# Performance work log

Hardware: AMD Instinct MI355X
Metric: run time of the kernel (lower is better)

The kernel has to match this reference:

```python
import jax, jax.numpy as jnp
import numpy as np

B, T, I, O = 128, 512, 700, 128  # batch, nb_steps, input_size, output_size
TIME_STEP, TAU_SYN, TAU_MEM, GAMMA_SHAPE = 1e-3, 10e-3, 20e-3, 3.0


def setup_inputs() -> dict:
    key = jax.random.key(0)
    k1, k2 = jax.random.split(key)
    inputs = jax.random.normal(k1, (B, T, I), dtype=jnp.float32)
    bound = 1.0 / np.sqrt(I)  # kaiming-uniform-like fan_in bound
    w = jax.random.uniform(k2, (I, O), minval=-bound, maxval=bound, dtype=jnp.float32)
    # heterogeneous per-neuron decay constants (het_ab=True), frozen params
    rng = np.random.default_rng(0)
    alpha = jnp.asarray(np.exp(-TIME_STEP / rng.gamma(GAMMA_SHAPE, TAU_SYN / GAMMA_SHAPE, (1, O))), dtype=jnp.float32)
    beta = jnp.asarray(np.exp(-TIME_STEP / rng.gamma(GAMMA_SHAPE, TAU_MEM / GAMMA_SHAPE, (1, O))), dtype=jnp.float32)
    return {"inputs": inputs, "w": w, "alpha": alpha, "beta": beta}


def reference(inputs, w, alpha, beta):
    # h: (B, T, O)
    h = jnp.einsum('btc,cd->btd', inputs, w)
    Bh, Th, Oh = h.shape
    zeros = jnp.zeros((Bh, Oh), dtype=h.dtype)
    one_minus_beta = 1.0 - beta  # beta is frozen, detach is a no-op here

    def step(carry, ht):
        syn, mem = carry
        new_syn = alpha * syn + ht
        new_mem = beta * mem + one_minus_beta * syn  # uses OLD syn
        return (new_syn, new_mem), (new_syn, new_mem)

    # scan over the first T-1 timesteps (time-major)
    h_tm = jnp.swapaxes(h[:, :Th - 1], 0, 1)  # (T-1, B, O)
    _, (syn_seq, mem_seq) = jax.lax.scan(step, (zeros, zeros), h_tm)
    syn_rec = jnp.concatenate([zeros[:, None], jnp.swapaxes(syn_seq, 0, 1)], axis=1)  # (B, T, O)
    mem_rec = jnp.concatenate([zeros[:, None], jnp.swapaxes(mem_seq, 0, 1)], axis=1)
    return (syn_rec, mem_rec)
```

## Files before the change

### kernel.cpp

```cpp
#include <hip/hip_runtime.h>
#include <hip/hip_bf16.h>
#include <stdint.h>

#define Bsz 128
#define Tn  512
#define In  700
#define On  128
#define Mn  (Bsz * Tn)
#define KP  704
#define NSEG 16
#define LSEG 32
#define BO   (Bsz * On)
#define NKT  22

using bf16x8 = __attribute__((ext_vector_type(8))) short;
using f32x4  = __attribute__((ext_vector_type(4))) float;

#define WAITVM(N) asm volatile("s_waitcnt vmcnt(" #N ")" ::: "memory")

__device__ __forceinline__ uint32_t f2bf(float f) {
  union { float f; uint32_t u; } v; v.f = f;
  return (v.u + 0x7fffu + ((v.u >> 16) & 1u)) >> 16;
}

__device__ __forceinline__ bf16x8 cvt8(float4 f0, float4 f1) {
  union { __hip_bfloat162 h2[4]; bf16x8 v; } u;
  u.h2[0] = __float22bfloat162_rn(make_float2(f0.x, f0.y));
  u.h2[1] = __float22bfloat162_rn(make_float2(f0.z, f0.w));
  u.h2[2] = __float22bfloat162_rn(make_float2(f1.x, f1.y));
  u.h2[3] = __float22bfloat162_rn(make_float2(f1.z, f1.w));
  return u.v;
}

__device__ __forceinline__ void gload16(const void* g, void* l) {
  __builtin_amdgcn_global_load_lds(
      (__attribute__((address_space(1))) void*)g,
      (__attribute__((address_space(3))) void*)l, 16, 0, 0);
}

__global__ void prep_wt(const float* __restrict__ w, ushort* __restrict__ w_t) {
  int idx = blockIdx.x * 256 + threadIdx.x;
  if (idx >= On * KP) return;
  int col = idx / KP, k = idx - col * KP;
  float v = (k < In) ? w[(size_t)k * On + col] : 0.0f;
  w_t[(size_t)col * KP + k] = (ushort)f2bf(v);
}

union SMU {
  struct {
    uint32_t A[3][4096];
    uint32_t B[3][2048];
  } db;
  float sc[128 * 132];
};

__global__ __launch_bounds__(256, 2) void gemm_h(
    const float* __restrict__ A,
    const ushort* __restrict__ Wt,
    float* __restrict__ H,
    float2* __restrict__ ep,
    const float* __restrict__ alpha, const float* __restrict__ beta)
{
  __shared__ __align__(16) SMU sm;

  const int tid  = threadIdx.x;
  const int bm   = blockIdx.x;
  const int lane = tid & 63;
  const int wid  = tid >> 6;
  const int wm   = wid >> 1, wn = wid & 1;
  const int l16  = lane & 15, lkb = lane >> 4;

  const int   o_ep = tid & 127;
  const float a_ep = alpha[o_ep];
  const float b_ep = beta[o_ep];
  WAITVM(0);
  __builtin_amdgcn_sched_barrier(0);

  f32x4 acc[4][4];
#pragma unroll
  for (int i = 0; i < 4; ++i)
#pragma unroll
    for (int n = 0; n < 4; ++n) acc[i][n] = (f32x4){0.f, 0.f, 0.f, 0.f};

  auto stage = [&](int bi, int kt) {
    const int k0 = kt * 32;
#pragma unroll
    for (int is = 0; is < 4; ++is) {
      const int q   = is * 256 + wid * 64 + lane;
      const int row = q >> 3, sl = q & 7;
      int gk = k0 + ((sl ^ (row & 7)) << 2);
      if (gk >= In) gk = k0;
      gload16(A + (size_t)(bm * 128 + row) * In + gk,
              &sm.db.A[bi][is * 1024 + wid * 256]);
    }
#pragma unroll
    for (int is = 0; is < 2; ++is) {
      const int q   = is * 256 + wid * 64 + lane;
      const int col = q >> 2, sl = q & 3;
      const int ks  = sl ^ ((col >> 1) & 3);
      gload16(Wt + (size_t)col * KP + k0 + ks * 8,
              &sm.db.B[bi][is * 1024 + wid * 256]);
    }
  };

  auto tile = [&](int kt, int cur) {
    __builtin_amdgcn_s_barrier();
    const float4* Af = (const float4*)sm.db.A[cur];
    const bf16x8* Bf = (const bf16x8*)sm.db.B[cur];
    bf16x8 af[4], bfr[4];
#pragma unroll
    for (int i = 0; i < 4; ++i) {
      const int row = wm * 64 + i * 16 + l16;
      const int s0  = (lkb * 2) ^ (row & 7);
      const int s1  = (lkb * 2 + 1) ^ (row & 7);
      af[i] = cvt8(Af[row * 8 + s0], Af[row * 8 + s1]);
    }
#pragma unroll
    for (int n = 0; n < 4; ++n) {
      const int col = wn * 64 + n * 16 + l16;
      bfr[n] = Bf[col * 4 + (lkb ^ ((col >> 1) & 3))];
    }
    asm volatile("s_waitcnt lgkmcnt(0)" ::: "memory");
    __builtin_amdgcn_s_barrier();
    if (kt + 3 < NKT) stage(cur, kt + 3);
#pragma unroll
    for (int i = 0; i < 4; ++i)
#pragma unroll
      for (int n = 0; n < 4; ++n)
        acc[i][n] = __builtin_amdgcn_mfma_f32_16x16x32_bf16(af[i], bfr[n], acc[i][n], 0, 0, 0);
  };

  stage(0, 0); stage(1, 1); stage(2, 2);
  {
    int cur = 0;
    for (int kt = 0; kt < NKT - 2; ++kt) {
      WAITVM(12);
      tile(kt, cur);
      cur = (cur == 2) ? 0 : cur + 1;
    }
    WAITVM(6);  tile(NKT - 2, (NKT - 2) % 3);
    WAITVM(0);  tile(NKT - 1, (NKT - 1) % 3);
  }

#pragma unroll
  for (int i = 0; i < 4; ++i)
#pragma unroll
    for (int n = 0; n < 4; ++n) {
      const int col = wn * 64 + n * 16 + l16;
#pragma unroll
      for (int r = 0; r < 4; ++r) {
        const int row = wm * 64 + i * 16 + lkb * 4 + r;
        sm.sc[row * 132 + col] = acc[i][n][r];
      }
    }
  __syncthreads();

  const size_t hbase = (size_t)bm * 128 * 128;
#pragma unroll
  for (int i2 = 0; i2 < 16; ++i2) {
    const int q = i2 * 256 + tid;
    const int row = q >> 5, v = q & 31;
    *(float4*)&H[hbase + row * 128 + v * 4] =
        *(const float4*)&sm.sc[row * 132 + v * 4];
  }

  if (ep) {
    const float a = a_ep, bt = b_ep, omb = 1.0f - b_ep;
    const int b = bm >> 2, seg0 = (bm & 3) * 4;
#pragma unroll
    for (int cc = 0; cc < 2; ++cc) {
      const int sl = (tid >> 7) + cc * 2;
      float S = 0.f, M = 0.f;
      const float* base = &sm.sc[(sl * 32) * 132 + o_ep];
#pragma unroll
      for (int t = 0; t < 32; ++t) {
        const float x = base[t * 132];
        M = fmaf(bt, M, omb * S);
        S = fmaf(a, S, x);
      }
      ep[(size_t)(seg0 + sl) * BO + b * On + o_ep] = make_float2(S, M);
    }
  }
}

__global__ __launch_bounds__(256) void scan_seg(
    float* __restrict__ syn, float* __restrict__ mem, const float2* __restrict__ ep,
    const float* __restrict__ alpha, const float* __restrict__ beta)
{
  const int cid = blockIdx.x * 256 + threadIdx.x;
  const int o2  = cid & 63;
  const int seg = (cid >> 6) & (NSEG - 1);
  const int b   = cid >> 10;
  const int o   = 2 * o2;

  const float2 al2 = *(const float2*)&alpha[o];
  const float2 be2 = *(const float2*)&beta[o];
  const float a0 = al2.x, a1 = al2.y, b0 = be2.x, b1 = be2.y;
  const float ob0 = 1.f - b0, ob1 = 1.f - b1;

  float aL0 = 1.f, bL0 = 1.f, cL0 = 0.f, aL1 = 1.f, bL1 = 1.f, cL1 = 0.f;
#pragma unroll
  for (int i = 0; i < LSEG; ++i) {
    cL0 = fmaf(b0, cL0, ob0 * aL0); aL0 *= a0; bL0 *= b0;
    cL1 = fmaf(b1, cL1, ob1 * aL1); aL1 *= a1; bL1 *= b1;
  }

  float S0 = 0.f, M0 = 0.f, S1 = 0.f, M1 = 0.f;
  for (int j = 0; j < seg; ++j) {
    const float4 E = *(const float4*)&ep[(size_t)j * BO + b * On + o];
    const float nS0 = fmaf(aL0, S0, E.x);
    M0 = fmaf(bL0, M0, fmaf(cL0, S0, E.y));
    S0 = nS0;
    const float nS1 = fmaf(aL1, S1, E.z);
    M1 = fmaf(bL1, M1, fmaf(cL1, S1, E.w));
    S1 = nS1;
  }

  float* hp = syn + ((size_t)b * Tn + seg * LSEG) * On + o;
  float* mp = mem + ((size_t)b * Tn + seg * LSEG) * On + o;
  float2 buf[8];
#pragma unroll
  for (int d = 0; d < 8; ++d) buf[d] = *(const float2*)&hp[d * On];
  for (int tb = 0; tb < LSEG; tb += 8) {
#pragma unroll
    for (int d = 0; d < 8; ++d) {
      const int t = tb + d;
      const float2 x = buf[d];
      if (t + 8 < LSEG) buf[d] = *(const float2*)&hp[(t + 8) * On];
      *(float2*)&hp[(size_t)t * On] = make_float2(S0, S1);
      *(float2*)&mp[(size_t)t * On] = make_float2(M0, M1);
      M0 = fmaf(b0, M0, ob0 * S0); S0 = fmaf(a0, S0, x.x);
      M1 = fmaf(b1, M1, ob1 * S1); S1 = fmaf(a1, S1, x.y);
    }
  }
}

__global__ __launch_bounds__(64) void scan_k(
    float* __restrict__ syn, float* __restrict__ mem,
    const float* __restrict__ alpha, const float* __restrict__ beta)
{
  const int b = blockIdx.x >> 1;
  const int o = ((blockIdx.x & 1) << 6) + threadIdx.x;
  const float a = alpha[o], bt = beta[o], omb = 1.0f - bt;
  float* hp = syn + (size_t)b * Tn * On + o;
  float* mp = mem + (size_t)b * Tn * On + o;
  float S = 0.f, M = 0.f;
  float buf[8];
#pragma unroll
  for (int d = 0; d < 8; ++d) buf[d] = hp[d * On];
  for (int tb = 0; tb < Tn; tb += 8) {
#pragma unroll
    for (int d = 0; d < 8; ++d) {
      const int t = tb + d;
      const float h_t = buf[d];
      if (t + 8 < Tn) buf[d] = hp[(t + 8) * On];
      hp[t * On] = S;
      mp[t * On] = M;
      const float nS = fmaf(a, S, h_t);
      M = fmaf(bt, M, omb * S);
      S = nS;
    }
  }
}

extern "C" void kernel_launch(void* const* d_in, const int* in_sizes, int n_in,
                              void* d_out, int out_size, void* d_ws, size_t ws_size,
                              hipStream_t stream) {
  const float* inputs = (const float*)d_in[0];
  const float* w      = (const float*)d_in[1];
  const float* alpha  = (const float*)d_in[2];
  const float* beta   = (const float*)d_in[3];

  float* syn = (float*)d_out;
  float* mem = syn + (size_t)Bsz * Tn * On;
  ushort* w_t = (ushort*)mem;

  const size_t ep_bytes = (size_t)NSEG * BO * sizeof(float2);
  float2* ep = (ws_size >= ep_bytes) ? (float2*)d_ws : nullptr;

  prep_wt<<<(On * KP + 255) / 256, 256, 0, stream>>>(w, w_t);
  gemm_h<<<Mn / 128, 256, 0, stream>>>(inputs, w_t, syn, ep, alpha, beta);

  if (ep) {
    scan_seg<<<(Bsz * NSEG * On / 2) / 256, 256, 0, stream>>>(syn, mem, ep, alpha, beta);
  } else {
    scan_k<<<Bsz * 2, 64, 0, stream>>>(syn, mem, alpha, beta);
  }
}
```

Baseline: 62.13 us.

## Store GEMM intermediate h as bf16 in workspace and scan from it

The GEMM now rounds its h tile to bf16 and writes it as packed bf16 to a workspace buffer instead of fp32 into the syn output. A new scan kernel reads the bf16 h, processes four output columns per thread, and writes syn and mem. The segment-boundary summaries are also computed from the rounded values, so the intermediate traffic for h is halved. In exchange, h carries bf16 rounding, which adds error to syn and mem, and the path needs a larger workspace.

```diff
diff --git a/kernel.cpp b/kernel.cpp
--- a/kernel.cpp
+++ b/kernel.cpp
@@ -22,6 +22,18 @@
   union { float f; uint32_t u; } v; v.f = f;
   return (v.u + 0x7fffu + ((v.u >> 16) & 1u)) >> 16;
 }
+__device__ __forceinline__ float bf16exact(float x) {
+  union { float f; uint32_t u; } v; v.f = x;
+  v.u = (v.u + 0x7fffu + ((v.u >> 16) & 1u)) & 0xFFFF0000u;
+  return v.f;
+}
+__device__ __forceinline__ float bf2f(ushort u) {
+  union { float f; uint32_t x; } v; v.x = ((uint32_t)u) << 16;
+  return v.f;
+}
+__device__ __forceinline__ uint32_t topbits(float x) {
+  union { float f; uint32_t u; } v; v.f = x; return v.u;
+}
 
 __device__ __forceinline__ bf16x8 cvt8(float4 f0, float4 f1) {
   union { __hip_bfloat162 h2[4]; bf16x8 v; } u;
@@ -54,10 +66,12 @@
   float sc[128 * 132];
 };
 
+template <bool HB16>
 __global__ __launch_bounds__(256, 2) void gemm_h(
     const float* __restrict__ A,
     const ushort* __restrict__ Wt,
-    float* __restrict__ H,
+    float* __restrict__ Hf,
+    ushort* __restrict__ Hb,
     float2* __restrict__ ep,
     const float* __restrict__ alpha, const float* __restrict__ beta)
 {
@@ -150,18 +164,36 @@
 #pragma unroll
       for (int r = 0; r < 4; ++r) {
         const int row = wm * 64 + i * 16 + lkb * 4 + r;
-        sm.sc[row * 132 + col] = acc[i][n][r];
+        float v = acc[i][n][r];
+        if constexpr (HB16) v = bf16exact(v);
+        sm.sc[row * 132 + col] = v;
       }
     }
   __syncthreads();
 
-  const size_t hbase = (size_t)bm * 128 * 128;
-#pragma unroll
-  for (int i2 = 0; i2 < 16; ++i2) {
-    const int q = i2 * 256 + tid;
-    const int row = q >> 5, v = q & 31;
-    *(float4*)&H[hbase + row * 128 + v * 4] =
-        *(const float4*)&sm.sc[row * 132 + v * 4];
+  if constexpr (HB16) {
+#pragma unroll
+    for (int i2 = 0; i2 < 8; ++i2) {
+      const int q = i2 * 256 + tid;
+      const int row = q >> 4, v8 = q & 15;
+      const float4 f0 = *(const float4*)&sm.sc[row * 132 + v8 * 8];
+      const float4 f1 = *(const float4*)&sm.sc[row * 132 + v8 * 8 + 4];
+      uint4 pk;
+      pk.x = (topbits(f0.x) >> 16) | (topbits(f0.y) & 0xFFFF0000u);
+      pk.y = (topbits(f0.z) >> 16) | (topbits(f0.w) & 0xFFFF0000u);
+      pk.z = (topbits(f1.x) >> 16) | (topbits(f1.y) & 0xFFFF0000u);
+      pk.w = (topbits(f1.z) >> 16) | (topbits(f1.w) & 0xFFFF0000u);
+      *(uint4*)&Hb[(size_t)(bm * 128 + row) * 128 + v8 * 8] = pk;
+    }
+  } else {
+    const size_t hbase = (size_t)bm * 128 * 128;
+#pragma unroll
+    for (int i2 = 0; i2 < 16; ++i2) {
+      const int q = i2 * 256 + tid;
+      const int row = q >> 5, v = q & 31;
+      *(float4*)&Hf[hbase + row * 128 + v * 4] =
+          *(const float4*)&sm.sc[row * 132 + v * 4];
+    }
   }
 
   if (ep) {
@@ -179,6 +211,72 @@
         S = fmaf(a, S, x);
       }
       ep[(size_t)(seg0 + sl) * BO + b * On + o_ep] = make_float2(S, M);
+    }
+  }
+}
+
+__global__ __launch_bounds__(256) void scan_seg16(
+    float* __restrict__ syn, float* __restrict__ mem,
+    const ushort* __restrict__ Hb, const float2* __restrict__ ep,
+    const float* __restrict__ alpha, const float* __restrict__ beta)
+{
+  const int cid = blockIdx.x * 256 + threadIdx.x;
+  const int o4  = cid & 31;
+  const int seg = (cid >> 5) & (NSEG - 1);
+  const int b   = cid >> 9;
+  const int o   = o4 * 4;
+
+  const float4 al = *(const float4*)&alpha[o];
+  const float4 be = *(const float4*)&beta[o];
+  float aa[4] = {al.x, al.y, al.z, al.w};
+  float bb[4] = {be.x, be.y, be.z, be.w};
+  float ob[4], aL[4], bL[4], cL[4], S[4], M[4];
+#pragma unroll
+  for (int c = 0; c < 4; ++c) {
+    ob[c] = 1.f - bb[c]; aL[c] = 1.f; bL[c] = 1.f; cL[c] = 0.f;
+    S[c] = 0.f; M[c] = 0.f;
+  }
+#pragma unroll
+  for (int i = 0; i < LSEG; ++i)
+#pragma unroll
+    for (int c = 0; c < 4; ++c) {
+      cL[c] = fmaf(bb[c], cL[c], ob[c] * aL[c]);
+      aL[c] *= aa[c]; bL[c] *= bb[c];
+    }
+
+  for (int j = 0; j < seg; ++j) {
+    const float4 E0 = *(const float4*)&ep[(size_t)j * BO + b * On + o];
+    const float4 E1 = *(const float4*)&ep[(size_t)j * BO + b * On + o + 2];
+    const float ex[4] = {E0.x, E0.z, E1.x, E1.z};
+    const float ey[4] = {E0.y, E0.w, E1.y, E1.w};
+#pragma unroll
+    for (int c = 0; c < 4; ++c) {
+      const float nS = fmaf(aL[c], S[c], ex[c]);
+      M[c] = fmaf(bL[c], M[c], fmaf(cL[c], S[c], ey[c]));
+      S[c] = nS;
+    }
+  }
+
+  const ushort* hp = Hb + ((size_t)b * Tn + seg * LSEG) * On + o;
+  float* sp = syn + ((size_t)b * Tn + seg * LSEG) * On + o;
+  float* mp = mem + ((size_t)b * Tn + seg * LSEG) * On + o;
+  ushort4 buf[4];
+#pragma unroll
+  for (int d = 0; d < 4; ++d) buf[d] = *(const ushort4*)&hp[d * On];
+  for (int tb = 0; tb < LSEG; tb += 4) {
+#pragma unroll
+    for (int d = 0; d < 4; ++d) {
+      const int t = tb + d;
+      const ushort4 u = buf[d];
+      if (t + 4 < LSEG) buf[d] = *(const ushort4*)&hp[(t + 4) * On];
+      *(float4*)&sp[(size_t)t * On] = make_float4(S[0], S[1], S[2], S[3]);
+      *(float4*)&mp[(size_t)t * On] = make_float4(M[0], M[1], M[2], M[3]);
+      const float x[4] = {bf2f(u.x), bf2f(u.y), bf2f(u.z), bf2f(u.w)};
+#pragma unroll
+      for (int c = 0; c < 4; ++c) {
+        M[c] = fmaf(bb[c], M[c], ob[c] * S[c]);
+        S[c] = fmaf(aa[c], S[c], x[c]);
+      }
     }
   }
 }
@@ -276,14 +374,21 @@
   ushort* w_t = (ushort*)mem;
 
   const size_t ep_bytes = (size_t)NSEG * BO * sizeof(float2);
-  float2* ep = (ws_size >= ep_bytes) ? (float2*)d_ws : nullptr;
+  const size_t hb_bytes = (size_t)Mn * On * sizeof(ushort);
 
   prep_wt<<<(On * KP + 255) / 256, 256, 0, stream>>>(w, w_t);
-  gemm_h<<<Mn / 128, 256, 0, stream>>>(inputs, w_t, syn, ep, alpha, beta);
-
-  if (ep) {
+
+  if (ws_size >= ep_bytes + hb_bytes) {
+    float2* ep = (float2*)d_ws;
+    ushort* hb = (ushort*)((char*)d_ws + ep_bytes);
+    gemm_h<true><<<Mn / 128, 256, 0, stream>>>(inputs, w_t, nullptr, hb, ep, alpha, beta);
+    scan_seg16<<<(Bsz * NSEG * On / 4) / 256, 256, 0, stream>>>(syn, mem, hb, ep, alpha, beta);
+  } else if (ws_size >= ep_bytes) {
+    float2* ep = (float2*)d_ws;
+    gemm_h<false><<<Mn / 128, 256, 0, stream>>>(inputs, w_t, syn, nullptr, ep, alpha, beta);
     scan_seg<<<(Bsz * NSEG * On / 2) / 256, 256, 0, stream>>>(syn, mem, ep, alpha, beta);
   } else {
+    gemm_h<false><<<Mn / 128, 256, 0, stream>>>(inputs, w_t, syn, nullptr, nullptr, alpha, beta);
     scan_k<<<Bsz * 2, 64, 0, stream>>>(syn, mem, alpha, beta);
   }
 }
```

Result: no change. 63.37 us (+2.0%).

## Load GEMM operands directly to registers and pass H as bf16 to the scan

Applied to the files above, without the earlier changes.

The GEMM drops the LDS triple-buffered global_load_lds staging and instead double-buffers A and W tiles in registers, with each wave computing 32 rows by all 128 columns. When the workspace is large enough, the intermediate H is rounded to bf16 and written to a workspace buffer instead of fp32 into the syn output. A new scan kernel then reads the half-size bf16 H. This cuts intermediate write and read traffic, at the cost of bf16 precision in the scan input and possibly weaker load coalescing or reuse in the GEMM without LDS sharing.

```diff
diff --git a/kernel.cpp b/kernel.cpp
--- a/kernel.cpp
+++ b/kernel.cpp
@@ -16,11 +16,20 @@
 using bf16x8 = __attribute__((ext_vector_type(8))) short;
 using f32x4  = __attribute__((ext_vector_type(4))) float;
 
-#define WAITVM(N) asm volatile("s_waitcnt vmcnt(" #N ")" ::: "memory")
-
 __device__ __forceinline__ uint32_t f2bf(float f) {
   union { float f; uint32_t u; } v; v.f = f;
   return (v.u + 0x7fffu + ((v.u >> 16) & 1u)) >> 16;
+}
+__device__ __forceinline__ float bf16exact(float x) {
+  union { float f; uint32_t u; } v; v.f = x;
+  v.u = (v.u + 0x7fffu + ((v.u >> 16) & 1u)) & 0xFFFF0000u;
+  return v.f;
+}
+__device__ __forceinline__ float bitsf(uint32_t u) {
+  union { float f; uint32_t x; } v; v.x = u; return v.f;
+}
+__device__ __forceinline__ uint32_t topbits(float x) {
+  union { float f; uint32_t u; } v; v.f = x; return v.u;
 }
 
 __device__ __forceinline__ bf16x8 cvt8(float4 f0, float4 f1) {
@@ -32,12 +41,6 @@
   return u.v;
 }
 
-__device__ __forceinline__ void gload16(const void* g, void* l) {
-  __builtin_amdgcn_global_load_lds(
-      (__attribute__((address_space(1))) void*)g,
-      (__attribute__((address_space(3))) void*)l, 16, 0, 0);
-}
-
 __global__ void prep_wt(const float* __restrict__ w, ushort* __restrict__ w_t) {
   int idx = blockIdx.x * 256 + threadIdx.x;
   if (idx >= On * KP) return;
@@ -46,122 +49,111 @@
   w_t[(size_t)col * KP + k] = (ushort)f2bf(v);
 }
 
-union SMU {
-  struct {
-    uint32_t A[3][4096];
-    uint32_t B[3][2048];
-  } db;
-  float sc[128 * 132];
-};
-
-__global__ __launch_bounds__(256, 2) void gemm_h(
+template <bool HB16>
+__global__ __launch_bounds__(256, 2) void gemm_h2(
     const float* __restrict__ A,
     const ushort* __restrict__ Wt,
-    float* __restrict__ H,
+    float* __restrict__ Hf,
+    ushort* __restrict__ Hb,
     float2* __restrict__ ep,
     const float* __restrict__ alpha, const float* __restrict__ beta)
 {
-  __shared__ __align__(16) SMU sm;
+  __shared__ float sc[128 * 132];
 
   const int tid  = threadIdx.x;
   const int bm   = blockIdx.x;
   const int lane = tid & 63;
-  const int wid  = tid >> 6;
-  const int wm   = wid >> 1, wn = wid & 1;
+  const int w    = tid >> 6;
   const int l16  = lane & 15, lkb = lane >> 4;
 
   const int   o_ep = tid & 127;
   const float a_ep = alpha[o_ep];
   const float b_ep = beta[o_ep];
-  WAITVM(0);
-  __builtin_amdgcn_sched_barrier(0);
-
-  f32x4 acc[4][4];
-#pragma unroll
-  for (int i = 0; i < 4; ++i)
-#pragma unroll
-    for (int n = 0; n < 4; ++n) acc[i][n] = (f32x4){0.f, 0.f, 0.f, 0.f};
-
-  auto stage = [&](int bi, int kt) {
+
+  const float*  ap0 = A + (size_t)(bm * 128 + w * 32 + l16) * In + lkb * 8;
+  const float*  ap1 = ap0 + (size_t)16 * In;
+  const ushort* wp  = Wt + (size_t)l16 * KP + lkb * 8;
+
+  f32x4 acc[2][8];
+#pragma unroll
+  for (int m = 0; m < 2; ++m)
+#pragma unroll
+    for (int n = 0; n < 8; ++n) acc[m][n] = (f32x4){0.f, 0.f, 0.f, 0.f};
+
+  struct Tile { float4 a00, a01, a10, a11; bf16x8 b[8]; };
+  auto loadT = [&](int kt, Tile& T) {
     const int k0 = kt * 32;
-#pragma unroll
-    for (int is = 0; is < 4; ++is) {
-      const int q   = is * 256 + wid * 64 + lane;
-      const int row = q >> 3, sl = q & 7;
-      int gk = k0 + ((sl ^ (row & 7)) << 2);
-      if (gk >= In) gk = k0;
-      gload16(A + (size_t)(bm * 128 + row) * In + gk,
-              &sm.db.A[bi][is * 1024 + wid * 256]);
-    }
-#pragma unroll
-    for (int is = 0; is < 2; ++is) {
-      const int q   = is * 256 + wid * 64 + lane;
-      const int col = q >> 2, sl = q & 3;
-      const int ks  = sl ^ ((col >> 1) & 3);
-      gload16(Wt + (size_t)col * KP + k0 + ks * 8,
-              &sm.db.B[bi][is * 1024 + wid * 256]);
-    }
+    const int gk = k0;
+    const int d2 = (k0 + lkb * 8 + 4 <= In - 4) ? 4 : (In - 4 - (k0 + lkb * 8));
+    T.a00 = *(const float4*)(ap0 + gk);
+    T.a01 = *(const float4*)(ap0 + gk + d2);
+    T.a10 = *(const float4*)(ap1 + gk);
+    T.a11 = *(const float4*)(ap1 + gk + d2);
+#pragma unroll
+    for (int n = 0; n < 8; ++n)
+      T.b[n] = *(const bf16x8*)(wp + (size_t)n * 16 * KP + k0);
   };
-
-  auto tile = [&](int kt, int cur) {
-    __builtin_amdgcn_s_barrier();
-    const float4* Af = (const float4*)sm.db.A[cur];
-    const bf16x8* Bf = (const bf16x8*)sm.db.B[cur];
-    bf16x8 af[4], bfr[4];
-#pragma unroll
-    for (int i = 0; i < 4; ++i) {
-      const int row = wm * 64 + i * 16 + l16;
-      const int s0  = (lkb * 2) ^ (row & 7);
-      const int s1  = (lkb * 2 + 1) ^ (row & 7);
-      af[i] = cvt8(Af[row * 8 + s0], Af[row * 8 + s1]);
-    }
-#pragma unroll
-    for (int n = 0; n < 4; ++n) {
-      const int col = wn * 64 + n * 16 + l16;
-      bfr[n] = Bf[col * 4 + (lkb ^ ((col >> 1) & 3))];
-    }
-    asm volatile("s_waitcnt lgkmcnt(0)" ::: "memory");
-    __builtin_amdgcn_s_barrier();
-    if (kt + 3 < NKT) stage(cur, kt + 3);
-#pragma unroll
-    for (int i = 0; i < 4; ++i)
-#pragma unroll
-      for (int n = 0; n < 4; ++n)
-        acc[i][n] = __builtin_amdgcn_mfma_f32_16x16x32_bf16(af[i], bfr[n], acc[i][n], 0, 0, 0);
+  auto compute = [&](const Tile& T) {
+    bf16x8 af0 = cvt8(T.a00, T.a01);
+    bf16x8 af1 = cvt8(T.a10, T.a11);
+#pragma unroll
+    for (int n = 0; n < 8; ++n) {
+      acc[0][n] = __builtin_amdgcn_mfma_f32_16x16x32_bf16(af0, T.b[n], acc[0][n], 0, 0, 0);
+      acc[1][n] = __builtin_amdgcn_mfma_f32_16x16x32_bf16(af1, T.b[n], acc[1][n], 0, 0, 0);
+    }
   };
 
-  stage(0, 0); stage(1, 1); stage(2, 2);
-  {
-    int cur = 0;
-    for (int kt = 0; kt < NKT - 2; ++kt) {
-      WAITVM(12);
-      tile(kt, cur);
-      cur = (cur == 2) ? 0 : cur + 1;
-    }
-    WAITVM(6);  tile(NKT - 2, (NKT - 2) % 3);
-    WAITVM(0);  tile(NKT - 1, (NKT - 1) % 3);
-  }
-
-#pragma unroll
-  for (int i = 0; i < 4; ++i)
-#pragma unroll
-    for (int n = 0; n < 4; ++n) {
-      const int col = wn * 64 + n * 16 + l16;
+  Tile R0, R1;
+  loadT(0, R0);
+#pragma unroll 1
+  for (int kt = 0; kt < NKT - 2; kt += 2) {
+    loadT(kt + 1, R1);
+    compute(R0);
+    loadT(kt + 2, R0);
+    compute(R1);
+  }
+  loadT(NKT - 1, R1);
+  compute(R0);
+  compute(R1);
+
+#pragma unroll
+  for (int m = 0; m < 2; ++m)
+#pragma unroll
+    for (int n = 0; n < 8; ++n) {
+      const int col = n * 16 + l16;
 #pragma unroll
       for (int r = 0; r < 4; ++r) {
-        const int row = wm * 64 + i * 16 + lkb * 4 + r;
-        sm.sc[row * 132 + col] = acc[i][n][r];
+        const int row = w * 32 + m * 16 + lkb * 4 + r;
+        float v = acc[m][n][r];
+        if constexpr (HB16) v = bf16exact(v);
+        sc[row * 132 + col] = v;
       }
     }
   __syncthreads();
 
-  const size_t hbase = (size_t)bm * 128 * 128;
-#pragma unroll
-  for (int i2 = 0; i2 < 16; ++i2) {
-    const int q = i2 * 256 + tid;
-    const int row = q >> 5, v = q & 31;
-    *(float4*)&H[hbase + row * 128 + v * 4] =
-        *(const float4*)&sm.sc[row * 132 + v * 4];
+  if constexpr (HB16) {
+#pragma unroll
+    for (int i2 = 0; i2 < 8; ++i2) {
+      const int q = i2 * 256 + tid;
+      const int row = q >> 4, v8 = q & 15;
+      const float4 f0 = *(const float4*)&sc[row * 132 + v8 * 8];
+      const float4 f1 = *(const float4*)&sc[row * 132 + v8 * 8 + 4];
+      uint4 pk;
+      pk.x = (topbits(f0.x) >> 16) | (topbits(f0.y) & 0xFFFF0000u);
+      pk.y = (topbits(f0.z) >> 16) | (topbits(f0.w) & 0xFFFF0000u);
+      pk.z = (topbits(f1.x) >> 16) | (topbits(f1.y) & 0xFFFF0000u);
+      pk.w = (topbits(f1.z) >> 16) | (topbits(f1.w) & 0xFFFF0000u);
+      *(uint4*)&Hb[(size_t)(bm * 128 + row) * 128 + v8 * 8] = pk;
+    }
+  } else {
+    const size_t hbase = (size_t)bm * 128 * 128;
+#pragma unroll
+    for (int i2 = 0; i2 < 16; ++i2) {
+      const int q = i2 * 256 + tid;
+      const int row = q >> 5, v = q & 31;
+      *(float4*)&Hf[hbase + row * 128 + v * 4] =
+          *(const float4*)&sc[row * 132 + v * 4];
+    }
   }
 
   if (ep) {
@@ -171,7 +163,7 @@
     for (int cc = 0; cc < 2; ++cc) {
       const int sl = (tid >> 7) + cc * 2;
       float S = 0.f, M = 0.f;
-      const float* base = &sm.sc[(sl * 32) * 132 + o_ep];
+      const float* base = &sc[(sl * 32) * 132 + o_ep];
 #pragma unroll
       for (int t = 0; t < 32; ++t) {
         const float x = base[t * 132];
@@ -179,6 +171,62 @@
         S = fmaf(a, S, x);
       }
       ep[(size_t)(seg0 + sl) * BO + b * On + o_ep] = make_float2(S, M);
+    }
+  }
+}
+
+__global__ __launch_bounds__(256) void scan_segb(
+    float* __restrict__ syn, float* __restrict__ mem,
+    const ushort* __restrict__ Hb, const float2* __restrict__ ep,
+    const float* __restrict__ alpha, const float* __restrict__ beta)
+{
+  const int cid = blockIdx.x * 256 + threadIdx.x;
+  const int o2  = cid & 63;
+  const int seg = (cid >> 6) & (NSEG - 1);
+  const int b   = cid >> 10;
+  const int o   = 2 * o2;
+
+  const float2 al2 = *(const float2*)&alpha[o];
+  const float2 be2 = *(const float2*)&beta[o];
+  const float a0 = al2.x, a1 = al2.y, b0 = be2.x, b1 = be2.y;
+  const float ob0 = 1.f - b0, ob1 = 1.f - b1;
+
+  float aL0 = 1.f, bL0 = 1.f, cL0 = 0.f, aL1 = 1.f, bL1 = 1.f, cL1 = 0.f;
+#pragma unroll
+  for (int i = 0; i < LSEG; ++i) {
+    cL0 = fmaf(b0, cL0, ob0 * aL0); aL0 *= a0; bL0 *= b0;
+    cL1 = fmaf(b1, cL1, ob1 * aL1); aL1 *= a1; bL1 *= b1;
+  }
+
+  float S0 = 0.f, M0 = 0.f, S1 = 0.f, M1 = 0.f;
+  for (int j = 0; j < seg; ++j) {
+    const float4 E = *(const float4*)&ep[(size_t)j * BO + b * On + o];
+    const float nS0 = fmaf(aL0, S0, E.x);
+    M0 = fmaf(bL0, M0, fmaf(cL0, S0, E.y));
+    S0 = nS0;
+    const float nS1 = fmaf(aL1, S1, E.z);
+    M1 = fmaf(bL1, M1, fmaf(cL1, S1, E.w));
+    S1 = nS1;
+  }
+
+  const ushort* hp = Hb + ((size_t)b * Tn + seg * LSEG) * On + o;
+  float* sp = syn + ((size_t)b * Tn + seg * LSEG) * On + o;
+  float* mp = mem + ((size_t)b * Tn + seg * LSEG) * On + o;
+  uint32_t buf[8];
+#pragma unroll
+  for (int d = 0; d < 8; ++d) buf[d] = *(const uint32_t*)&hp[d * On];
+  for (int tb = 0; tb < LSEG; tb += 8) {
+#pragma unroll
+    for (int d = 0; d < 8; ++d) {
+      const int t = tb + d;
+      const uint32_t u = buf[d];
+      if (t + 8 < LSEG) buf[d] = *(const uint32_t*)&hp[(t + 8) * On];
+      *(float2*)&sp[(size_t)t * On] = make_float2(S0, S1);
+      *(float2*)&mp[(size_t)t * On] = make_float2(M0, M1);
+      const float x0 = bitsf(u << 16);
+      const float x1 = bitsf(u & 0xFFFF0000u);
+      M0 = fmaf(b0, M0, ob0 * S0); S0 = fmaf(a0, S0, x0);
+      M1 = fmaf(b1, M1, ob1 * S1); S1 = fmaf(a1, S1, x1);
     }
   }
 }
@@ -276,14 +324,21 @@
   ushort* w_t = (ushort*)mem;
 
   const size_t ep_bytes = (size_t)NSEG * BO * sizeof(float2);
-  float2* ep = (ws_size >= ep_bytes) ? (float2*)d_ws : nullptr;
+  const size_t hb_bytes = (size_t)Mn * On * sizeof(ushort);
 
   prep_wt<<<(On * KP + 255) / 256, 256, 0, stream>>>(w, w_t);
-  gemm_h<<<Mn / 128, 256, 0, stream>>>(inputs, w_t, syn, ep, alpha, beta);
-
-  if (ep) {
+
+  if (ws_size >= ep_bytes + hb_bytes) {
+    float2* ep = (float2*)d_ws;
+    ushort* hb = (ushort*)((char*)d_ws + ep_bytes);
+    gemm_h2<true><<<Mn / 128, 256, 0, stream>>>(inputs, w_t, nullptr, hb, ep, alpha, beta);
+    scan_segb<<<(Bsz * NSEG * On / 2) / 256, 256, 0, stream>>>(syn, mem, hb, ep, alpha, beta);
+  } else if (ws_size >= ep_bytes) {
+    float2* ep = (float2*)d_ws;
+    gemm_h2<false><<<Mn / 128, 256, 0, stream>>>(inputs, w_t, syn, nullptr, ep, alpha, beta);
     scan_seg<<<(Bsz * NSEG * On / 2) / 256, 256, 0, stream>>>(syn, mem, ep, alpha, beta);
   } else {
+    gemm_h2<false><<<Mn / 128, 256, 0, stream>>>(inputs, w_t, syn, nullptr, nullptr, alpha, beta);
     scan_k<<<Bsz * 2, 64, 0, stream>>>(syn, mem, alpha, beta);
   }
 }
```

Result: slower. 101.6 us (+63.6%).
